# Performance work log

Measured on AMD Instinct MI355X. Metric: run time of the kernel, lower is better.

Reference implementation:

```python
import jax, jax.numpy as jnp
import numpy as np

MARGIN = 0.2
NUM_CLASSES = 55
B, D = 8192, 512


def setup_inputs() -> dict:
    key = jax.random.key(0)
    k1, k2, k3 = jax.random.split(key, 3)
    inputs = jax.random.normal(k1, (B, D), dtype=jnp.float32)
    targets = jax.random.randint(k2, (B,), 0, NUM_CLASSES, dtype=jnp.int64)
    centers = jax.random.normal(k3, (NUM_CLASSES, D), dtype=jnp.float32)
    return {"inputs": inputs, "targets": targets, "centers": centers}


def reference(inputs, targets, centers):
    # Gather the center for each target: centers_batch[j] = centers[targets[j]]  -> [B, D]
    centers_batch = centers[targets]
    # Pairwise distance dist[i, j] = ||inputs[i] - centers[targets[j]]||  -> [B, B]
    # (quadratic expansion avoids the original's [B, B, D] intermediate)
    sq = (
        jnp.sum(inputs * inputs, axis=1)[:, None]
        + jnp.sum(centers_batch * centers_batch, axis=1)[None, :]
        - 2.0 * (inputs @ centers_batch.T)
    )
    dist = jnp.sqrt(jnp.clip(sq, 1e-12, None))
    # mask[i, j] = (targets[i] == targets[j])
    mask = targets[:, None] == targets[None, :]
    # hardest positive (max over same-class cols), hardest negative (min over other-class cols)
    dist_ap = jnp.max(jnp.where(mask, dist, -jnp.inf), axis=1)  # [B]
    dist_an = jnp.min(jnp.where(mask, jnp.inf, dist), axis=1)   # [B]
    # MarginRankingLoss with y = 1: mean(max(0, dist_ap - dist_an + margin))
    loss = jnp.mean(jnp.maximum(dist_ap - dist_an + MARGIN, 0.0))
    prec = jnp.mean((dist_an > dist_ap).astype(jnp.float32))
    return loss, prec
```

## Files before the change

kernel.cpp:

```cpp
#include <hip/hip_runtime.h>
#include <hip/hip_bf16.h>
#include <math.h>

#define NB 8192
#define ND 512
#define NC 55
#define TCL_MARGIN 0.2f

typedef __attribute__((ext_vector_type(8))) short short8;
typedef __attribute__((ext_vector_type(4))) float f32x4;

__device__ __forceinline__ short bf16h(float v) {
  union { __hip_bfloat16 b; short s; } u;
  u.b = __float2bfloat16(v);
  return u.s;
}
__device__ __forceinline__ short bf16lo(float v, short hi) {
  const float fhi = __uint_as_float(((unsigned)(unsigned short)hi) << 16);
  return bf16h(v - fhi);
}

__global__ __launch_bounds__(256)
void tcl_fused(const float* __restrict__ x, const int* __restrict__ tg,
               const float* __restrict__ cen, float* __restrict__ ws,
               float* __restrict__ out) {
  __shared__ f32x4 accL[3][4][64];
  __shared__ float xnL[4][16];
  __shared__ float cnL[4][4][16];
  __shared__ float wsumF[4];
  __shared__ int wsumI[4];

  const int t = threadIdx.x;
  const int l = t & 63;
  const int w = t >> 6;
  const int row0 = blockIdx.x * 16;
  const int rlo = l & 15;
  const int kgE = (l >> 4) * 8;

  const unsigned P = *(const unsigned*)((const char*)ws + 4096);
  const unsigned tag27 = (P + 0x00C0FFEEu) & 0x07FFFFFFu;

  const float* xr = x + (row0 + rlo) * ND;
  float4 va[4][2];
#pragma unroll
  for (int ksl = 0; ksl < 4; ++ksl) {
    const int k0 = (w * 4 + ksl) * 32 + kgE;
    va[ksl][0] = *(const float4*)(xr + k0);
    va[ksl][1] = *(const float4*)(xr + k0 + 4);
  }

  unsigned long long pm = 0ull;
  if (w == 0) {
    const int4* tg4 = (const int4*)tg;
#pragma unroll
    for (int g = 0; g < 8; ++g) {
      int4 v = tg4[l + g * 64];
      pm |= (1ull << v.x) | (1ull << v.y) | (1ull << v.z) | (1ull << v.w);
    }
#pragma unroll
    for (int off = 32; off; off >>= 1) pm |= __shfl_xor(pm, off);
  }

  float xn = 0.f;
#pragma unroll
  for (int ksl = 0; ksl < 4; ++ksl) {
    float4 a = va[ksl][0], b = va[ksl][1];
    xn = fmaf(a.x, a.x, xn); xn = fmaf(a.y, a.y, xn);
    xn = fmaf(a.z, a.z, xn); xn = fmaf(a.w, a.w, xn);
    xn = fmaf(b.x, b.x, xn); xn = fmaf(b.y, b.y, xn);
    xn = fmaf(b.z, b.z, xn); xn = fmaf(b.w, b.w, xn);
  }
  xn += __shfl_xor(xn, 16);
  xn += __shfl_xor(xn, 32);
  if (l < 16) xnL[w][l] = xn;

  const float* cb[4];
#pragma unroll
  for (int ct = 0; ct < 4; ++ct) {
    int col = ct * 16 + rlo;
    if (col > NC - 1) col = NC - 1;
    cb[ct] = cen + col * ND + kgE;
  }

  f32x4 acc[4] = {{0.f,0.f,0.f,0.f},{0.f,0.f,0.f,0.f},{0.f,0.f,0.f,0.f},{0.f,0.f,0.f,0.f}};
  float cnp[4] = {0.f, 0.f, 0.f, 0.f};
#pragma unroll
  for (int ksl = 0; ksl < 4; ++ksl) {
    short8 ah, al;
    {
      float4 a = va[ksl][0], b = va[ksl][1];
      ah[0] = bf16h(a.x); ah[1] = bf16h(a.y); ah[2] = bf16h(a.z); ah[3] = bf16h(a.w);
      ah[4] = bf16h(b.x); ah[5] = bf16h(b.y); ah[6] = bf16h(b.z); ah[7] = bf16h(b.w);
      al[0] = bf16lo(a.x, ah[0]); al[1] = bf16lo(a.y, ah[1]);
      al[2] = bf16lo(a.z, ah[2]); al[3] = bf16lo(a.w, ah[3]);
      al[4] = bf16lo(b.x, ah[4]); al[5] = bf16lo(b.y, ah[5]);
      al[6] = bf16lo(b.z, ah[6]); al[7] = bf16lo(b.w, ah[7]);
    }
    const int ko = (w * 4 + ksl) * 32;
#pragma unroll
    for (int ct = 0; ct < 4; ++ct) {
      float4 b0 = *(const float4*)(cb[ct] + ko);
      float4 b1 = *(const float4*)(cb[ct] + ko + 4);
      float c = cnp[ct];
      c = fmaf(b0.x, b0.x, c); c = fmaf(b0.y, b0.y, c);
      c = fmaf(b0.z, b0.z, c); c = fmaf(b0.w, b0.w, c);
      c = fmaf(b1.x, b1.x, c); c = fmaf(b1.y, b1.y, c);
      c = fmaf(b1.z, b1.z, c); c = fmaf(b1.w, b1.w, c);
      cnp[ct] = c;
      short8 bh;
      bh[0] = bf16h(b0.x); bh[1] = bf16h(b0.y); bh[2] = bf16h(b0.z); bh[3] = bf16h(b0.w);
      bh[4] = bf16h(b1.x); bh[5] = bf16h(b1.y); bh[6] = bf16h(b1.z); bh[7] = bf16h(b1.w);
      acc[ct] = __builtin_amdgcn_mfma_f32_16x16x32_bf16(ah, bh, acc[ct], 0, 0, 0);
      acc[ct] = __builtin_amdgcn_mfma_f32_16x16x32_bf16(al, bh, acc[ct], 0, 0, 0);
    }
  }

#pragma unroll
  for (int ct = 0; ct < 4; ++ct) {
    float c = cnp[ct];
    c += __shfl_xor(c, 16);
    c += __shfl_xor(c, 32);
    if (l < 16) cnL[w][ct][l] = c;
  }

  if (w) {
#pragma unroll
    for (int ct = 0; ct < 4; ++ct) accL[w - 1][ct][l] = acc[ct];
  }
  __syncthreads();

  if (w == 0) {
#pragma unroll
    for (int wv = 0; wv < 3; ++wv)
#pragma unroll
      for (int ct = 0; ct < 4; ++ct) {
        f32x4 p = accL[wv][ct][l];
        acc[ct][0] += p[0]; acc[ct][1] += p[1];
        acc[ct][2] += p[2]; acc[ct][3] += p[3];
      }
    float xns = (l < 16) ? (xnL[0][l] + xnL[1][l] + xnL[2][l] + xnL[3][l]) : 0.f;

    float cn[4];
    bool cv[4];
#pragma unroll
    for (int ct = 0; ct < 4; ++ct) {
      cn[ct] = cnL[0][ct][rlo] + cnL[1][ct][rlo] + cnL[2][ct][rlo] + cnL[3][ct][rlo];
      const int col = ct * 16 + rlo;
      cv[ct] = (col < NC) && (((pm >> col) & 1ull) != 0ull);
    }

    const int tgl = (l < 16) ? tg[row0 + l] : 0;
    const int g4 = (l >> 4) * 4;
    float wl = 0.f;
    int wp = 0;
#pragma unroll
    for (int r = 0; r < 4; ++r) {
      const int row = g4 + r;
      const int tjr = __shfl(tgl, row);
      const float xnr = __shfl(xns, row);
      const float s0 = fmaxf(xnr + cn[0] - 2.0f * acc[0][r], 1e-12f);
      const float s1 = fmaxf(xnr + cn[1] - 2.0f * acc[1][r], 1e-12f);
      const float s2 = fmaxf(xnr + cn[2] - 2.0f * acc[2][r], 1e-12f);
      const float s3 = fmaxf(xnr + cn[3] - 2.0f * acc[3][r], 1e-12f);
      const int c2 = tjr >> 4;
      const float dsel = (c2 == 0) ? s0 : (c2 == 1) ? s1 : (c2 == 2) ? s2 : s3;
      const float apq = __shfl(dsel, (l & 48) | (tjr & 15));
      const float INF = __builtin_inff();
      float m0 = (cv[0] && (rlo != tjr)) ? s0 : INF;
      float m1 = (cv[1] && (16 + rlo != tjr)) ? s1 : INF;
      float m2 = (cv[2] && (32 + rlo != tjr)) ? s2 : INF;
      float m3 = (cv[3] && (48 + rlo != tjr)) ? s3 : INF;
      float mn = fminf(fminf(m0, m1), fminf(m2, m3));
      mn = fminf(mn, __shfl_xor(mn, 1));
      mn = fminf(mn, __shfl_xor(mn, 2));
      mn = fminf(mn, __shfl_xor(mn, 4));
      mn = fminf(mn, __shfl_xor(mn, 8));
      if (rlo == 0) {
        const float ap = sqrtf(apq), an = sqrtf(mn);
        wl += fmaxf(ap - an + TCL_MARGIN, 0.f);
        wp += (an > ap) ? 1 : 0;
      }
    }
    wl += __shfl_xor(wl, 16); wl += __shfl_xor(wl, 32);
    wp += __shfl_xor(wp, 16); wp += __shfl_xor(wp, 32);

    if (l == 0) {
      const unsigned lo = (tag27 << 5) | (unsigned)(wp & 31);
      const unsigned long long sv =
          ((unsigned long long)__float_as_uint(wl) << 32) | (unsigned long long)lo;
      __hip_atomic_store((unsigned long long*)ws + blockIdx.x, sv,
                         __ATOMIC_RELAXED, __HIP_MEMORY_SCOPE_AGENT);
    }
  }

  if (blockIdx.x != 0) return;

  {
    float Ls = 0.f;
    int Ps = 0;
#pragma unroll
    for (int s = 0; s < 2; ++s) {
      const int idx = t + s * 256;
      unsigned long long v;
      for (;;) {
        v = __hip_atomic_load((const unsigned long long*)ws + idx,
                              __ATOMIC_RELAXED, __HIP_MEMORY_SCOPE_AGENT);
        if (((unsigned)v >> 5) == tag27) break;
        __builtin_amdgcn_s_sleep(1);
      }
      Ls += __uint_as_float((unsigned)(v >> 32));
      Ps += (int)((unsigned)v & 31u);
    }
#pragma unroll
    for (int off = 32; off; off >>= 1) {
      Ls += __shfl_xor(Ls, off);
      Ps += __shfl_xor(Ps, off);
    }
    if (l == 0) { wsumF[w] = Ls; wsumI[w] = Ps; }
    __syncthreads();
    if (t == 0) {
      const float lsum = wsumF[0] + wsumF[1] + wsumF[2] + wsumF[3];
      const int psum = wsumI[0] + wsumI[1] + wsumI[2] + wsumI[3];
      out[0] = lsum * (1.0f / NB);
      out[1] = (float)psum * (1.0f / NB);
      *(unsigned*)((char*)ws + 4096) = P + 1;
    }
  }
}

extern "C" void kernel_launch(void* const* d_in, const int* in_sizes, int n_in,
                              void* d_out, int out_size, void* d_ws, size_t ws_size,
                              hipStream_t stream) {
  const float* x = (const float*)d_in[0];
  const int* tg = (const int*)d_in[1];
  const float* cen = (const float*)d_in[2];
  float* out = (float*)d_out;
  float* ws = (float*)d_ws;

  tcl_fused<<<dim3(NB / 16), dim3(256), 0, stream>>>(x, tg, cen, ws, out);
}
```

Measured before the change: 18.12 us.

## Process 32 rows per block with 8 waves splitting K

Each block now handles 32 rows instead of 16, using 512 threads whose 8 waves each cover a 64-wide K slice for two 16-row tiles. Every center fragment loaded is reused for two row tiles, which halves center traffic per row. The grid drops from 512 to 256 blocks, so block 0's final spin-wait reads half as many partial slots. The cost is a bigger shared-memory reduction across 8 waves, an extra block barrier, and fewer blocks to spread across CUs.

```diff
diff --git a/kernel.cpp b/kernel.cpp
--- a/kernel.cpp
+++ b/kernel.cpp
@@ -20,38 +20,44 @@
   return bf16h(v - fhi);
 }
 
-__global__ __launch_bounds__(256)
+__global__ __launch_bounds__(512)
 void tcl_fused(const float* __restrict__ x, const int* __restrict__ tg,
                const float* __restrict__ cen, float* __restrict__ ws,
                float* __restrict__ out) {
-  __shared__ f32x4 accL[3][4][64];
-  __shared__ float xnL[4][16];
-  __shared__ float cnL[4][4][16];
-  __shared__ float wsumF[4];
-  __shared__ int wsumI[4];
+  __shared__ f32x4 accL[2][8][4][64];
+  __shared__ float xnL[8][2][16];
+  __shared__ float cnL[8][4][16];
+  __shared__ unsigned long long pmL;
+  __shared__ float eL[2];
+  __shared__ int eP[2];
+  __shared__ float wsumF[8];
+  __shared__ int wsumI[8];
 
   const int t = threadIdx.x;
   const int l = t & 63;
   const int w = t >> 6;
-  const int row0 = blockIdx.x * 16;
+  const int row0 = blockIdx.x * 32;
   const int rlo = l & 15;
   const int kgE = (l >> 4) * 8;
 
   const unsigned P = *(const unsigned*)((const char*)ws + 4096);
-  const unsigned tag27 = (P + 0x00C0FFEEu) & 0x07FFFFFFu;
-
-  const float* xr = x + (row0 + rlo) * ND;
-  float4 va[4][2];
-#pragma unroll
-  for (int ksl = 0; ksl < 4; ++ksl) {
-    const int k0 = (w * 4 + ksl) * 32 + kgE;
-    va[ksl][0] = *(const float4*)(xr + k0);
-    va[ksl][1] = *(const float4*)(xr + k0 + 4);
-  }
-
-  unsigned long long pm = 0ull;
+  const unsigned tag26 = (P + 0x00C0FFEEu) & 0x03FFFFFFu;
+
+  const float* xr0 = x + (row0 + rlo) * ND;
+  const float* xr1 = xr0 + 16 * ND;
+  float4 va[2][2][2];
+#pragma unroll
+  for (int ksl = 0; ksl < 2; ++ksl) {
+    const int k0 = w * 64 + ksl * 32 + kgE;
+    va[0][ksl][0] = *(const float4*)(xr0 + k0);
+    va[0][ksl][1] = *(const float4*)(xr0 + k0 + 4);
+    va[1][ksl][0] = *(const float4*)(xr1 + k0);
+    va[1][ksl][1] = *(const float4*)(xr1 + k0 + 4);
+  }
+
   if (w == 0) {
     const int4* tg4 = (const int4*)tg;
+    unsigned long long pm = 0ull;
 #pragma unroll
     for (int g = 0; g < 8; ++g) {
       int4 v = tg4[l + g * 64];
@@ -59,20 +65,28 @@
     }
 #pragma unroll
     for (int off = 32; off; off >>= 1) pm |= __shfl_xor(pm, off);
-  }
-
-  float xn = 0.f;
-#pragma unroll
-  for (int ksl = 0; ksl < 4; ++ksl) {
-    float4 a = va[ksl][0], b = va[ksl][1];
-    xn = fmaf(a.x, a.x, xn); xn = fmaf(a.y, a.y, xn);
-    xn = fmaf(a.z, a.z, xn); xn = fmaf(a.w, a.w, xn);
-    xn = fmaf(b.x, b.x, xn); xn = fmaf(b.y, b.y, xn);
-    xn = fmaf(b.z, b.z, xn); xn = fmaf(b.w, b.w, xn);
-  }
-  xn += __shfl_xor(xn, 16);
-  xn += __shfl_xor(xn, 32);
-  if (l < 16) xnL[w][l] = xn;
+    if (l == 0) pmL = pm;
+  }
+
+  {
+    float xn0 = 0.f, xn1 = 0.f;
+#pragma unroll
+    for (int ksl = 0; ksl < 2; ++ksl) {
+      float4 a0 = va[0][ksl][0], b0 = va[0][ksl][1];
+      float4 a1 = va[1][ksl][0], b1 = va[1][ksl][1];
+      xn0 = fmaf(a0.x, a0.x, xn0); xn0 = fmaf(a0.y, a0.y, xn0);
+      xn0 = fmaf(a0.z, a0.z, xn0); xn0 = fmaf(a0.w, a0.w, xn0);
+      xn0 = fmaf(b0.x, b0.x, xn0); xn0 = fmaf(b0.y, b0.y, xn0);
+      xn0 = fmaf(b0.z, b0.z, xn0); xn0 = fmaf(b0.w, b0.w, xn0);
+      xn1 = fmaf(a1.x, a1.x, xn1); xn1 = fmaf(a1.y, a1.y, xn1);
+      xn1 = fmaf(a1.z, a1.z, xn1); xn1 = fmaf(a1.w, a1.w, xn1);
+      xn1 = fmaf(b1.x, b1.x, xn1); xn1 = fmaf(b1.y, b1.y, xn1);
+      xn1 = fmaf(b1.z, b1.z, xn1); xn1 = fmaf(b1.w, b1.w, xn1);
+    }
+    xn0 += __shfl_xor(xn0, 16); xn0 += __shfl_xor(xn0, 32);
+    xn1 += __shfl_xor(xn1, 16); xn1 += __shfl_xor(xn1, 32);
+    if (l < 16) { xnL[w][0][l] = xn0; xnL[w][1][l] = xn1; }
+  }
 
   const float* cb[4];
 #pragma unroll
@@ -82,21 +96,31 @@
     cb[ct] = cen + col * ND + kgE;
   }
 
-  f32x4 acc[4] = {{0.f,0.f,0.f,0.f},{0.f,0.f,0.f,0.f},{0.f,0.f,0.f,0.f},{0.f,0.f,0.f,0.f}};
+  f32x4 acc0[4] = {{0.f,0.f,0.f,0.f},{0.f,0.f,0.f,0.f},{0.f,0.f,0.f,0.f},{0.f,0.f,0.f,0.f}};
+  f32x4 acc1[4] = {{0.f,0.f,0.f,0.f},{0.f,0.f,0.f,0.f},{0.f,0.f,0.f,0.f},{0.f,0.f,0.f,0.f}};
   float cnp[4] = {0.f, 0.f, 0.f, 0.f};
 #pragma unroll
-  for (int ksl = 0; ksl < 4; ++ksl) {
-    short8 ah, al;
+  for (int ksl = 0; ksl < 2; ++ksl) {
+    short8 ah0, al0, ah1, al1;
     {
-      float4 a = va[ksl][0], b = va[ksl][1];
-      ah[0] = bf16h(a.x); ah[1] = bf16h(a.y); ah[2] = bf16h(a.z); ah[3] = bf16h(a.w);
-      ah[4] = bf16h(b.x); ah[5] = bf16h(b.y); ah[6] = bf16h(b.z); ah[7] = bf16h(b.w);
-      al[0] = bf16lo(a.x, ah[0]); al[1] = bf16lo(a.y, ah[1]);
-      al[2] = bf16lo(a.z, ah[2]); al[3] = bf16lo(a.w, ah[3]);
-      al[4] = bf16lo(b.x, ah[4]); al[5] = bf16lo(b.y, ah[5]);
-      al[6] = bf16lo(b.z, ah[6]); al[7] = bf16lo(b.w, ah[7]);
-    }
-    const int ko = (w * 4 + ksl) * 32;
+      float4 a = va[0][ksl][0], b = va[0][ksl][1];
+      ah0[0] = bf16h(a.x); ah0[1] = bf16h(a.y); ah0[2] = bf16h(a.z); ah0[3] = bf16h(a.w);
+      ah0[4] = bf16h(b.x); ah0[5] = bf16h(b.y); ah0[6] = bf16h(b.z); ah0[7] = bf16h(b.w);
+      al0[0] = bf16lo(a.x, ah0[0]); al0[1] = bf16lo(a.y, ah0[1]);
+      al0[2] = bf16lo(a.z, ah0[2]); al0[3] = bf16lo(a.w, ah0[3]);
+      al0[4] = bf16lo(b.x, ah0[4]); al0[5] = bf16lo(b.y, ah0[5]);
+      al0[6] = bf16lo(b.z, ah0[6]); al0[7] = bf16lo(b.w, ah0[7]);
+    }
+    {
+      float4 a = va[1][ksl][0], b = va[1][ksl][1];
+      ah1[0] = bf16h(a.x); ah1[1] = bf16h(a.y); ah1[2] = bf16h(a.z); ah1[3] = bf16h(a.w);
+      ah1[4] = bf16h(b.x); ah1[5] = bf16h(b.y); ah1[6] = bf16h(b.z); ah1[7] = bf16h(b.w);
+      al1[0] = bf16lo(a.x, ah1[0]); al1[1] = bf16lo(a.y, ah1[1]);
+      al1[2] = bf16lo(a.z, ah1[2]); al1[3] = bf16lo(a.w, ah1[3]);
+      al1[4] = bf16lo(b.x, ah1[4]); al1[5] = bf16lo(b.y, ah1[5]);
+      al1[6] = bf16lo(b.z, ah1[6]); al1[7] = bf16lo(b.w, ah1[7]);
+    }
+    const int ko = w * 64 + ksl * 32;
 #pragma unroll
     for (int ct = 0; ct < 4; ++ct) {
       float4 b0 = *(const float4*)(cb[ct] + ko);
@@ -110,8 +134,10 @@
       short8 bh;
       bh[0] = bf16h(b0.x); bh[1] = bf16h(b0.y); bh[2] = bf16h(b0.z); bh[3] = bf16h(b0.w);
       bh[4] = bf16h(b1.x); bh[5] = bf16h(b1.y); bh[6] = bf16h(b1.z); bh[7] = bf16h(b1.w);
-      acc[ct] = __builtin_amdgcn_mfma_f32_16x16x32_bf16(ah, bh, acc[ct], 0, 0, 0);
-      acc[ct] = __builtin_amdgcn_mfma_f32_16x16x32_bf16(al, bh, acc[ct], 0, 0, 0);
+      acc0[ct] = __builtin_amdgcn_mfma_f32_16x16x32_bf16(ah0, bh, acc0[ct], 0, 0, 0);
+      acc0[ct] = __builtin_amdgcn_mfma_f32_16x16x32_bf16(al0, bh, acc0[ct], 0, 0, 0);
+      acc1[ct] = __builtin_amdgcn_mfma_f32_16x16x32_bf16(ah1, bh, acc1[ct], 0, 0, 0);
+      acc1[ct] = __builtin_amdgcn_mfma_f32_16x16x32_bf16(al1, bh, acc1[ct], 0, 0, 0);
     }
   }
 
@@ -121,35 +147,38 @@
     c += __shfl_xor(c, 16);
     c += __shfl_xor(c, 32);
     if (l < 16) cnL[w][ct][l] = c;
-  }
-
-  if (w) {
-#pragma unroll
-    for (int ct = 0; ct < 4; ++ct) accL[w - 1][ct][l] = acc[ct];
+    accL[0][w][ct][l] = acc0[ct];
+    accL[1][w][ct][l] = acc1[ct];
   }
   __syncthreads();
 
-  if (w == 0) {
-#pragma unroll
-    for (int wv = 0; wv < 3; ++wv)
-#pragma unroll
-      for (int ct = 0; ct < 4; ++ct) {
-        f32x4 p = accL[wv][ct][l];
-        acc[ct][0] += p[0]; acc[ct][1] += p[1];
-        acc[ct][2] += p[2]; acc[ct][3] += p[3];
-      }
-    float xns = (l < 16) ? (xnL[0][l] + xnL[1][l] + xnL[2][l] + xnL[3][l]) : 0.f;
-
+  if (w < 2) {
+    f32x4 acc[4];
     float cn[4];
     bool cv[4];
+    const unsigned long long pmv = pmL;
 #pragma unroll
     for (int ct = 0; ct < 4; ++ct) {
-      cn[ct] = cnL[0][ct][rlo] + cnL[1][ct][rlo] + cnL[2][ct][rlo] + cnL[3][ct][rlo];
+      f32x4 s = accL[w][0][ct][l];
+#pragma unroll
+      for (int wv = 1; wv < 8; ++wv) {
+        f32x4 p = accL[w][wv][ct][l];
+        s[0] += p[0]; s[1] += p[1]; s[2] += p[2]; s[3] += p[3];
+      }
+      acc[ct] = s;
+      float c = cnL[0][ct][rlo];
+#pragma unroll
+      for (int wv = 1; wv < 8; ++wv) c += cnL[wv][ct][rlo];
+      cn[ct] = c;
       const int col = ct * 16 + rlo;
-      cv[ct] = (col < NC) && (((pm >> col) & 1ull) != 0ull);
-    }
-
-    const int tgl = (l < 16) ? tg[row0 + l] : 0;
+      cv[ct] = (col < NC) && (((pmv >> col) & 1ull) != 0ull);
+    }
+    float xns = 0.f;
+    if (l < 16) {
+#pragma unroll
+      for (int wv = 0; wv < 8; ++wv) xns += xnL[wv][w][l];
+    }
+    const int tgl = (l < 16) ? tg[row0 + w * 16 + l] : 0;
     const int g4 = (l >> 4) * 4;
     float wl = 0.f;
     int wp = 0;
@@ -183,14 +212,18 @@
     }
     wl += __shfl_xor(wl, 16); wl += __shfl_xor(wl, 32);
     wp += __shfl_xor(wp, 16); wp += __shfl_xor(wp, 32);
-
-    if (l == 0) {
-      const unsigned lo = (tag27 << 5) | (unsigned)(wp & 31);
-      const unsigned long long sv =
-          ((unsigned long long)__float_as_uint(wl) << 32) | (unsigned long long)lo;
-      __hip_atomic_store((unsigned long long*)ws + blockIdx.x, sv,
-                         __ATOMIC_RELAXED, __HIP_MEMORY_SCOPE_AGENT);
-    }
+    if (l == 0) { eL[w] = wl; eP[w] = wp; }
+  }
+  __syncthreads();
+
+  if (t == 0) {
+    const float wlb = eL[0] + eL[1];
+    const unsigned wpb = (unsigned)(eP[0] + eP[1]);
+    const unsigned lo = (tag26 << 6) | (wpb & 63u);
+    const unsigned long long sv =
+        ((unsigned long long)__float_as_uint(wlb) << 32) | (unsigned long long)lo;
+    __hip_atomic_store((unsigned long long*)ws + blockIdx.x, sv,
+                       __ATOMIC_RELAXED, __HIP_MEMORY_SCOPE_AGENT);
   }
 
   if (blockIdx.x != 0) return;
@@ -198,18 +231,16 @@
   {
     float Ls = 0.f;
     int Ps = 0;
-#pragma unroll
-    for (int s = 0; s < 2; ++s) {
-      const int idx = t + s * 256;
+    if (t < 256) {
       unsigned long long v;
       for (;;) {
-        v = __hip_atomic_load((const unsigned long long*)ws + idx,
+        v = __hip_atomic_load((const unsigned long long*)ws + t,
                               __ATOMIC_RELAXED, __HIP_MEMORY_SCOPE_AGENT);
-        if (((unsigned)v >> 5) == tag27) break;
+        if (((unsigned)v >> 6) == tag26) break;
         __builtin_amdgcn_s_sleep(1);
       }
-      Ls += __uint_as_float((unsigned)(v >> 32));
-      Ps += (int)((unsigned)v & 31u);
+      Ls = __uint_as_float((unsigned)(v >> 32));
+      Ps = (int)((unsigned)v & 63u);
     }
 #pragma unroll
     for (int off = 32; off; off >>= 1) {
@@ -219,8 +250,10 @@
     if (l == 0) { wsumF[w] = Ls; wsumI[w] = Ps; }
     __syncthreads();
     if (t == 0) {
-      const float lsum = wsumF[0] + wsumF[1] + wsumF[2] + wsumF[3];
-      const int psum = wsumI[0] + wsumI[1] + wsumI[2] + wsumI[3];
+      float lsum = 0.f;
+      int psum = 0;
+#pragma unroll
+      for (int wv = 0; wv < 8; ++wv) { lsum += wsumF[wv]; psum += wsumI[wv]; }
       out[0] = lsum * (1.0f / NB);
       out[1] = (float)psum * (1.0f / NB);
       *(unsigned*)((char*)ws + 4096) = P + 1;
@@ -237,5 +270,5 @@
   float* out = (float*)d_out;
   float* ws = (float*)d_ws;
 
-  tcl_fused<<<dim3(NB / 16), dim3(256), 0, stream>>>(x, tg, cen, ws, out);
-}
+  tcl_fused<<<dim3(NB / 32), dim3(512), 0, stream>>>(x, tg, cen, ws, out);
+}
```

Result: faster. 15.19 us (-16.2%).
